# Kernel optimization log

Measured on AMD Instinct MI355X. Metric: run time of the kernel, lower is better.

## Reference

```python
import jax, jax.numpy as jnp
import numpy as np


def setup_inputs() -> dict:
    key = jax.random.key(0)
    ks = jax.random.split(key, 8)
    N, DIN, DOUT = 8192, 1024, 1024
    s = 1.0 / np.sqrt(DIN)
    return {
        "gAB": jax.random.normal(ks[0], (N, DIN), dtype=jnp.float32),
        "gAG": jax.random.normal(ks[1], (N, DIN), dtype=jnp.float32),
        "Wab": jax.random.normal(ks[2], (DIN, DOUT), dtype=jnp.float32) * s,
        "Wag": jax.random.normal(ks[3], (DIN, DOUT), dtype=jnp.float32) * s,
        "bab": jax.random.normal(ks[4], (DOUT,), dtype=jnp.float32) * 0.01,
        "bag": jax.random.normal(ks[5], (DOUT,), dtype=jnp.float32) * 0.01,
        "sAB": jax.random.normal(ks[6], (N, DOUT), dtype=jnp.float32),
        "sAG": jax.random.normal(ks[7], (N, DOUT), dtype=jnp.float32),
    }


def reference(gAB, gAG, Wab, Wag, bab, bag, sAB, sAG) -> jnp.ndarray:
    # project() per encoder (Linear): [N, DIN] @ [DIN, DOUT] + b
    pAB = gAB @ Wab + bab  # [N, DOUT]
    pAG = gAG @ Wag + bag  # [N, DOUT]
    # torch.diag(pAB @ pAG.T) == row-wise dot product (avoids O(N^2 d) waste)
    h1 = jnp.sum(pAB * pAG, axis=1, keepdims=True)  # [N, 1]
    h2 = jnp.sum(sAB * sAG, axis=1, keepdims=True)  # [N, 1]
    # mean over concatenated (h1, h2) columns, keepdim=True
    h = jnp.mean(jnp.concatenate([h1, h2], axis=1), axis=1, keepdims=True)  # [N, 1]
    return h
```

## Files before the change

kernel.cpp:

```cpp
#include <hip/hip_runtime.h>
#include <hip/hip_bf16.h>
#include <stdint.h>

typedef __attribute__((ext_vector_type(8))) short bf16x8;
typedef __attribute__((ext_vector_type(4))) float f32x4;

#define DIN 1024
#define NROWS 8192

__device__ __forceinline__ unsigned short f2bf(float f) {
    union { float f; unsigned u; } v; v.f = f;
    unsigned r = v.u + 0x7FFFu + ((v.u >> 16) & 1u);
    return (unsigned short)(r >> 16);
}

__device__ __forceinline__ int fswz(int r) { return (r ^ (r >> 2)) & 3; }

__device__ __forceinline__ size_t swz_byte(int R, int col) {
    return ((size_t)R * DIN + (col & ~31)) * 2 + (size_t)((((col >> 3) & 3) ^ fswz(R)) << 4) + (size_t)((col & 7) * 2);
}

__device__ __forceinline__ void gload_lds16(const void* g, void* l) {
    __builtin_amdgcn_global_load_lds(
        (const __attribute__((address_space(1))) unsigned*)g,
        (__attribute__((address_space(3))) unsigned*)l, 16, 0, 0);
}

__global__ __launch_bounds__(256) void prep_kernel(const float* __restrict__ Wab,
                                                   const float* __restrict__ Wag,
                                                   const float* __restrict__ bab,
                                                   const float* __restrict__ bag,
                                                   float* __restrict__ ws_f,
                                                   unsigned short* __restrict__ Whab,
                                                   unsigned short* __restrict__ Whag) {
    int b = blockIdx.x;
    int wave = threadIdx.x >> 6, lane = threadIdx.x & 63;
    if (b == 256) {
        if (wave == 0) {
            float acc = 0.f;
            for (int j = lane; j < DIN; j += 64) acc += bab[j] * bag[j];
            for (int off = 32; off; off >>= 1) acc += __shfl_xor(acc, off);
            if (lane == 0) ws_f[2048] = acc;
        }
        return;
    }
    int r = b * 4 + wave;
    int fr = fswz(r);
    {
        const float* wrow = Wab + (size_t)r * DIN;
        char* hrow = (char*)Whab + (size_t)r * DIN * 2;
        float acc = 0.f;
#pragma unroll
        for (int it = 0; it < 4; ++it) {
            int col = it * 256 + lane * 4;
            float4 w = *reinterpret_cast<const float4*>(wrow + col);
            float4 bv = *reinterpret_cast<const float4*>(bag + col);
            acc += w.x * bv.x + w.y * bv.y + w.z * bv.z + w.w * bv.w;
            ushort4 h; h.x = f2bf(w.x); h.y = f2bf(w.y); h.z = f2bf(w.z); h.w = f2bf(w.w);
            *reinterpret_cast<ushort4*>(hrow + (col & ~31) * 2 + ((((col >> 3) & 3) ^ fr) << 4) + (col & 7) * 2) = h;
        }
        for (int off = 32; off; off >>= 1) acc += __shfl_xor(acc, off);
        if (lane == 0) ws_f[r] = acc;
    }
    {
        const float* wrow = Wag + (size_t)r * DIN;
        char* hrow = (char*)Whag + (size_t)r * DIN * 2;
        float acc = 0.f;
#pragma unroll
        for (int it = 0; it < 4; ++it) {
            int col = it * 256 + lane * 4;
            float4 w = *reinterpret_cast<const float4*>(wrow + col);
            float4 bv = *reinterpret_cast<const float4*>(bab + col);
            acc += w.x * bv.x + w.y * bv.y + w.z * bv.z + w.w * bv.w;
            ushort4 h; h.x = f2bf(w.x); h.y = f2bf(w.y); h.z = f2bf(w.z); h.w = f2bf(w.w);
            *reinterpret_cast<ushort4*>(hrow + (col & ~31) * 2 + ((((col >> 3) & 3) ^ fr) << 4) + (col & 7) * 2) = h;
        }
        for (int off = 32; off; off >>= 1) acc += __shfl_xor(acc, off);
        if (lane == 0) ws_f[1024 + r] = acc;
    }
}

__global__ __launch_bounds__(512) void mt_kernel(const unsigned short* __restrict__ Whag,
                                                 const unsigned short* __restrict__ Whab,
                                                 unsigned short* __restrict__ Mt) {
    __shared__ unsigned short sm[2][2][2][2048];
    int tid = threadIdx.x;
    int wave = tid >> 6, grp = wave >> 2, w4 = wave & 3;
    int lane = tid & 63, kg = lane >> 4, cl = lane & 15;
    int wr = w4 >> 1, wc = w4 & 1;
    int br = blockIdx.x >> 4, bc = blockIdx.x & 15;
    int u = tid & 255, urow = u >> 2, uchunk = u & 3;

    const char* Abase = (const char*)Whag + ((size_t)(br * 64 + urow) * DIN + grp * 512) * 2 + uchunk * 16;
    const char* Bbase = (const char*)Whab + ((size_t)(bc * 64 + urow) * DIN + grp * 512) * 2 + uchunk * 16;

    int offA[2], offB[2];
#pragma unroll
    for (int m = 0; m < 2; ++m) { int row = wr * 32 + m * 16 + cl; offA[m] = row * 32 + ((kg ^ fswz(row)) << 3); }
#pragma unroll
    for (int n = 0; n < 2; ++n) { int row = wc * 32 + n * 16 + cl; offB[n] = row * 32 + ((kg ^ fswz(row)) << 3); }

    f32x4 acc[2][2] = {};
    gload_lds16(Abase, &sm[grp][0][0][u * 8]);
    gload_lds16(Bbase, &sm[grp][0][1][u * 8]);
    __syncthreads();
    for (int t = 0; t < 16; ++t) {
        int p = t & 1;
        if (t < 15) {
            gload_lds16(Abase + (t + 1) * 64, &sm[grp][p ^ 1][0][u * 8]);
            gload_lds16(Bbase + (t + 1) * 64, &sm[grp][p ^ 1][1][u * 8]);
        }
        bf16x8 af[2], bfr[2];
#pragma unroll
        for (int m = 0; m < 2; ++m) af[m] = *reinterpret_cast<const bf16x8*>(&sm[grp][p][0][offA[m]]);
#pragma unroll
        for (int n = 0; n < 2; ++n) bfr[n] = *reinterpret_cast<const bf16x8*>(&sm[grp][p][1][offB[n]]);
#pragma unroll
        for (int m = 0; m < 2; ++m)
#pragma unroll
            for (int n = 0; n < 2; ++n)
                acc[m][n] = __builtin_amdgcn_mfma_f32_16x16x32_bf16(af[m], bfr[n], acc[m][n], 0, 0, 0);
        __syncthreads();
    }
    float* red = (float*)sm;
    if (grp == 1) {
#pragma unroll
        for (int m = 0; m < 2; ++m)
#pragma unroll
            for (int n = 0; n < 2; ++n)
#pragma unroll
                for (int j = 0; j < 4; ++j)
                    red[(wr * 32 + m * 16 + kg * 4 + j) * 68 + wc * 32 + n * 16 + cl] = acc[m][n][j];
    }
    __syncthreads();
    if (grp == 0) {
#pragma unroll
        for (int m = 0; m < 2; ++m)
#pragma unroll
            for (int n = 0; n < 2; ++n)
#pragma unroll
                for (int j = 0; j < 4; ++j) {
                    int rl = wr * 32 + m * 16 + kg * 4 + j, cll = wc * 32 + n * 16 + cl;
                    float v = acc[m][n][j] + red[rl * 68 + cll];
                    int R = br * 64 + rl, C = bc * 64 + cll;
                    *(unsigned short*)((char*)Mt + swz_byte(R, C & ~3) + (C & 3) * 2) = f2bf(v);
                }
    }
}

template <int KSPLIT>
__global__ __launch_bounds__(256, 4) void gemm_fused(const float* __restrict__ gAB,
                                                     const float* __restrict__ gAG,
                                                     const float* __restrict__ sAB,
                                                     const float* __restrict__ sAG,
                                                     const unsigned short* __restrict__ Mt,
                                                     const float* __restrict__ ws_f,
                                                     float* __restrict__ out) {
    __shared__ unsigned short lds_a[2][128 * 32];
    __shared__ unsigned short lds_b[2][128 * 32];
    constexpr int KLEN = DIN / KSPLIT;
    constexpr int NSTEP = KLEN / 32;
    int b = blockIdx.x;
    int x = b & 7, s = b >> 3;
    int rblk = x + 8 * (s & 7);
    int u2 = s >> 3;
    int ks = u2 & (KSPLIT - 1);
    int cblk = u2 / KSPLIT;
    int tid = threadIdx.x, wave = tid >> 6, lane = tid & 63;
    int wr = wave >> 1, wc = wave & 1;
    int kg = lane >> 4, cl = lane & 15;
    int row0 = rblk * 128, col0 = cblk * 128;

    int offA[4], offB[4];
#pragma unroll
    for (int m = 0; m < 4; ++m) { int row = wr * 64 + m * 16 + cl; offA[m] = row * 32 + ((kg ^ fswz(row)) << 3); }
#pragma unroll
    for (int n = 0; n < 4; ++n) { int row = wc * 64 + n * 16 + cl; offB[n] = row * 32 + ((kg ^ fswz(row)) << 3); }

    size_t kofs = (size_t)(ks * KLEN);
    const char* Bb = (const char*)Mt + ((size_t)col0 * DIN + kofs) * 2;
    int u0 = tid, u1 = tid + 256;
    size_t b0 = (size_t)(u0 >> 2) * (DIN * 2) + (u0 & 3) * 16;
    size_t b1 = (size_t)(u1 >> 2) * (DIN * 2) + (u1 & 3) * 16;
    const float* Abase = gAB + (size_t)row0 * DIN + kofs;

    f32x4 acc[4][4] = {};
    float4 ra[4];

    gload_lds16(Bb + b0, (char*)&lds_b[0][0] + u0 * 16);
    gload_lds16(Bb + b1, (char*)&lds_b[0][0] + u1 * 16);
#pragma unroll
    for (int it = 0; it < 4; ++it) {
        int u = tid + it * 256;
        ra[it] = *reinterpret_cast<const float4*>(Abase + (size_t)(u >> 3) * DIN + (u & 7) * 4);
    }
#pragma unroll
    for (int it = 0; it < 4; ++it) {
        int u = tid + it * 256, row = u >> 3, c4 = u & 7;
        ushort4 h; h.x = f2bf(ra[it].x); h.y = f2bf(ra[it].y); h.z = f2bf(ra[it].z); h.w = f2bf(ra[it].w);
        *reinterpret_cast<ushort4*>((char*)&lds_a[0][0] + row * 64 + ((((c4 >> 1) ^ fswz(row))) << 4) + (c4 & 1) * 8) = h;
    }
    __syncthreads();

    for (int t = 0; t < NSTEP; ++t) {
        int p = t & 1;
        if (t < NSTEP - 1) {
#pragma unroll
            for (int it = 0; it < 4; ++it) {
                int u = tid + it * 256;
                ra[it] = *reinterpret_cast<const float4*>(Abase + (size_t)(u >> 3) * DIN + (t + 1) * 32 + (u & 7) * 4);
            }
            gload_lds16(Bb + b0 + (t + 1) * 64, (char*)&lds_b[p ^ 1][0] + u0 * 16);
            gload_lds16(Bb + b1 + (t + 1) * 64, (char*)&lds_b[p ^ 1][0] + u1 * 16);
        }
        bf16x8 af[4], bfr[4];
#pragma unroll
        for (int m = 0; m < 4; ++m) af[m] = *reinterpret_cast<const bf16x8*>(&lds_a[p][offA[m]]);
#pragma unroll
        for (int n = 0; n < 4; ++n) bfr[n] = *reinterpret_cast<const bf16x8*>(&lds_b[p][offB[n]]);
#pragma unroll
        for (int m = 0; m < 4; ++m)
#pragma unroll
            for (int n = 0; n < 4; ++n)
                acc[m][n] = __builtin_amdgcn_mfma_f32_16x16x32_bf16(af[m], bfr[n], acc[m][n], 0, 0, 0);
        if (t < NSTEP - 1) {
#pragma unroll
            for (int it = 0; it < 4; ++it) {
                int u = tid + it * 256, row = u >> 3, c4 = u & 7;
                ushort4 h; h.x = f2bf(ra[it].x); h.y = f2bf(ra[it].y); h.z = f2bf(ra[it].z); h.w = f2bf(ra[it].w);
                *reinterpret_cast<ushort4*>((char*)&lds_a[p ^ 1][0] + row * 64 + ((((c4 >> 1) ^ fswz(row))) << 4) + (c4 & 1) * 8) = h;
            }
        }
        __syncthreads();
    }

    const float* vab = ws_f;
    const float* vag = ws_f + 1024;
    float cbias = ws_f[2048];
#pragma unroll
    for (int m = 0; m < 4; ++m)
#pragma unroll
        for (int j = 0; j < 4; ++j) {
            int row = row0 + wr * 64 + m * 16 + kg * 4 + j;
            const float* gr = gAG + (size_t)row * DIN;
            float t = 0.f;
#pragma unroll
            for (int n = 0; n < 4; ++n) {
                int col = col0 + wc * 64 + n * 16 + cl;
                float addv = (ks == 0) ? vag[col] : 0.f;
                t += gr[col] * (acc[m][n][j] + addv);
            }
            if (ks == 0) {
                const float* gar = gAB + (size_t)row * DIN;
                const float* sar = sAB + (size_t)row * DIN;
                const float* sgr = sAG + (size_t)row * DIN;
#pragma unroll
                for (int n = 0; n < 4; ++n) {
                    int col = col0 + wc * 64 + n * 16 + cl;
                    t += gar[col] * vab[col] + sar[col] * sgr[col];
                }
            }
            t += __shfl_xor(t, 1);
            t += __shfl_xor(t, 2);
            t += __shfl_xor(t, 4);
            t += __shfl_xor(t, 8);
            if (cl == 0) {
                float add = (ks == 0 && cblk == 0 && wc == 0) ? cbias : 0.f;
                atomicAdd(out + row, 0.5f * (t + add));
            }
        }
}

extern "C" void kernel_launch(void* const* d_in, const int* in_sizes, int n_in,
                              void* d_out, int out_size, void* d_ws, size_t ws_size,
                              hipStream_t stream) {
    const float* gAB = (const float*)d_in[0];
    const float* gAG = (const float*)d_in[1];
    const float* Wab = (const float*)d_in[2];
    const float* Wag = (const float*)d_in[3];
    const float* bab = (const float*)d_in[4];
    const float* bag = (const float*)d_in[5];
    const float* sAB = (const float*)d_in[6];
    const float* sAG = (const float*)d_in[7];
    float* out = (float*)d_out;

    float* ws_f = (float*)d_ws;
    char* base = (char*)d_ws + 16384;
    unsigned short* Mt = (unsigned short*)base;
    unsigned short* Whag = (unsigned short*)(base + (size_t)2 * 1024 * 1024);
    unsigned short* Whab = (unsigned short*)(base + (size_t)4 * 1024 * 1024);

    hipMemsetAsync(d_out, 0, (size_t)out_size * sizeof(float), stream);
    prep_kernel<<<257, 256, 0, stream>>>(Wab, Wag, bab, bag, ws_f, Whab, Whag);
    mt_kernel<<<256, 512, 0, stream>>>(Whag, Whab, Mt);
    gemm_fused<2><<<1024, 256, 0, stream>>>(gAB, gAG, sAB, sAG, Mt, ws_f, out);
}
```

Baseline: 70.45 us.

## Split row-dot and bias terms into dedicated blocks of a merged GEMM kernel

Adds 256 extra blocks to the fused GEMM launch. Each extra block streams rows of gAB, sAB and sAG with coalesced float4 loads and computes the sAB·sAG dot plus the gAB·vab bias term per row. The GEMM epilogue no longer does these scattered per-lane loads for the ks==0 tiles, which removes load imbalance between the K-split halves and cuts strided global reads. Occupancy hint raised from 4 to 5 blocks per SM; this risks register spills, and the streaming blocks compete for bandwidth with the GEMM blocks.

```diff
diff --git a/kernel.cpp b/kernel.cpp
--- a/kernel.cpp
+++ b/kernel.cpp
@@ -148,25 +148,56 @@
     }
 }
 
-template <int KSPLIT>
-__global__ __launch_bounds__(256, 4) void gemm_fused(const float* __restrict__ gAB,
-                                                     const float* __restrict__ gAG,
-                                                     const float* __restrict__ sAB,
-                                                     const float* __restrict__ sAG,
-                                                     const unsigned short* __restrict__ Mt,
-                                                     const float* __restrict__ ws_f,
-                                                     float* __restrict__ out) {
+__global__ __launch_bounds__(256, 5) void mega_kernel(const float* __restrict__ gAB,
+                                                      const float* __restrict__ gAG,
+                                                      const float* __restrict__ sAB,
+                                                      const float* __restrict__ sAG,
+                                                      const unsigned short* __restrict__ Mt,
+                                                      const float* __restrict__ ws_f,
+                                                      float* __restrict__ out) {
     __shared__ unsigned short lds_a[2][128 * 32];
     __shared__ unsigned short lds_b[2][128 * 32];
+    int b = blockIdx.x;
+    int tid = threadIdx.x, wave = tid >> 6, lane = tid & 63;
+
+    if (b < 256) {
+        float cbias = ws_f[2048];
+        float4 vb[4];
+#pragma unroll
+        for (int cc = 0; cc < 4; ++cc)
+            vb[cc] = *reinterpret_cast<const float4*>(ws_f + cc * 256 + lane * 4);
+        int row_base = b * 32 + wave * 8;
+        for (int rr = 0; rr < 8; ++rr) {
+            int row = row_base + rr;
+            const float* ga = gAB + (size_t)row * DIN;
+            const float* sa = sAB + (size_t)row * DIN;
+            const float* sg = sAG + (size_t)row * DIN;
+            float acc = 0.f;
+#pragma unroll
+            for (int cc = 0; cc < 4; ++cc) {
+                int col = cc * 256 + lane * 4;
+                float4 a = *reinterpret_cast<const float4*>(ga + col);
+                float4 x = *reinterpret_cast<const float4*>(sa + col);
+                float4 y = *reinterpret_cast<const float4*>(sg + col);
+                acc += x.x * y.x + x.y * y.y + x.z * y.z + x.w * y.w;
+                acc += a.x * vb[cc].x + a.y * vb[cc].y + a.z * vb[cc].z + a.w * vb[cc].w;
+            }
+#pragma unroll
+            for (int off = 32; off; off >>= 1) acc += __shfl_xor(acc, off);
+            if (lane == 0) atomicAdd(out + row, 0.5f * (acc + cbias));
+        }
+        return;
+    }
+
+    constexpr int KSPLIT = 2;
     constexpr int KLEN = DIN / KSPLIT;
     constexpr int NSTEP = KLEN / 32;
-    int b = blockIdx.x;
-    int x = b & 7, s = b >> 3;
+    int g = b - 256;
+    int x = g & 7, s = g >> 3;
     int rblk = x + 8 * (s & 7);
     int u2 = s >> 3;
     int ks = u2 & (KSPLIT - 1);
     int cblk = u2 / KSPLIT;
-    int tid = threadIdx.x, wave = tid >> 6, lane = tid & 63;
     int wr = wave >> 1, wc = wave & 1;
     int kg = lane >> 4, cl = lane & 15;
     int row0 = rblk * 128, col0 = cblk * 128;
@@ -234,9 +265,7 @@
         __syncthreads();
     }
 
-    const float* vab = ws_f;
     const float* vag = ws_f + 1024;
-    float cbias = ws_f[2048];
 #pragma unroll
     for (int m = 0; m < 4; ++m)
 #pragma unroll
@@ -250,24 +279,11 @@
                 float addv = (ks == 0) ? vag[col] : 0.f;
                 t += gr[col] * (acc[m][n][j] + addv);
             }
-            if (ks == 0) {
-                const float* gar = gAB + (size_t)row * DIN;
-                const float* sar = sAB + (size_t)row * DIN;
-                const float* sgr = sAG + (size_t)row * DIN;
-#pragma unroll
-                for (int n = 0; n < 4; ++n) {
-                    int col = col0 + wc * 64 + n * 16 + cl;
-                    t += gar[col] * vab[col] + sar[col] * sgr[col];
-                }
-            }
             t += __shfl_xor(t, 1);
             t += __shfl_xor(t, 2);
             t += __shfl_xor(t, 4);
             t += __shfl_xor(t, 8);
-            if (cl == 0) {
-                float add = (ks == 0 && cblk == 0 && wc == 0) ? cbias : 0.f;
-                atomicAdd(out + row, 0.5f * (t + add));
-            }
+            if (cl == 0) atomicAdd(out + row, 0.5f * t);
         }
 }
 
@@ -293,5 +309,5 @@
     hipMemsetAsync(d_out, 0, (size_t)out_size * sizeof(float), stream);
     prep_kernel<<<257, 256, 0, stream>>>(Wab, Wag, bab, bag, ws_f, Whab, Whag);
     mt_kernel<<<256, 512, 0, stream>>>(Whag, Whab, Mt);
-    gemm_fused<2><<<1024, 256, 0, stream>>>(gAB, gAG, sAB, sAG, Mt, ws_f, out);
-}
+    mega_kernel<<<1280, 256, 0, stream>>>(gAB, gAG, sAB, sAG, Mt, ws_f, out);
+}
```

Result: slower. 112.1 us (+59.1%).

## Fuse bf16 weight conversion into Mt GEMM and move bias/sAB·sAG terms into main loop

Applied to the files above, without the earlier changes.

Drops the separate bf16 copies of Wab/Wag: prep now only computes bias-projection vectors, and mt_kernel reads fp32 weights, converts them in registers and writes them to LDS. The main GEMM switches Mt to an 8-way XOR swizzle with a matching B staging pattern. It computes gAB·vab during the A conversion and sAB·sAG per column slice inside the K loop, reduced through LDS atomics. This removes the epilogue's scattered strided loads of gAB/sAB/sAG and the extra weight-conversion traffic. In exchange, the main loop carries more per-iteration global loads and the kernel adds LDS atomics.

```diff
diff --git a/kernel.cpp b/kernel.cpp
--- a/kernel.cpp
+++ b/kernel.cpp
@@ -14,10 +14,10 @@
     return (unsigned short)(r >> 16);
 }
 
-__device__ __forceinline__ int fswz(int r) { return (r ^ (r >> 2)) & 3; }
-
-__device__ __forceinline__ size_t swz_byte(int R, int col) {
-    return ((size_t)R * DIN + (col & ~31)) * 2 + (size_t)((((col >> 3) & 3) ^ fswz(R)) << 4) + (size_t)((col & 7) * 2);
+__device__ __forceinline__ size_t swz8_byte(int R, int c) {
+    return ((size_t)R * DIN + (size_t)(c & ~63)) * 2
+         + (size_t)(((((c >> 3) & 7) ^ (R & 7)) << 4))
+         + (size_t)((c & 7) * 2);
 }
 
 __device__ __forceinline__ void gload_lds16(const void* g, void* l) {
@@ -30,9 +30,7 @@
                                                    const float* __restrict__ Wag,
                                                    const float* __restrict__ bab,
                                                    const float* __restrict__ bag,
-                                                   float* __restrict__ ws_f,
-                                                   unsigned short* __restrict__ Whab,
-                                                   unsigned short* __restrict__ Whag) {
+                                                   float* __restrict__ ws_f) {
     int b = blockIdx.x;
     int wave = threadIdx.x >> 6, lane = threadIdx.x & 63;
     if (b == 256) {
@@ -45,43 +43,26 @@
         return;
     }
     int r = b * 4 + wave;
-    int fr = fswz(r);
-    {
-        const float* wrow = Wab + (size_t)r * DIN;
-        char* hrow = (char*)Whab + (size_t)r * DIN * 2;
-        float acc = 0.f;
-#pragma unroll
-        for (int it = 0; it < 4; ++it) {
-            int col = it * 256 + lane * 4;
-            float4 w = *reinterpret_cast<const float4*>(wrow + col);
-            float4 bv = *reinterpret_cast<const float4*>(bag + col);
-            acc += w.x * bv.x + w.y * bv.y + w.z * bv.z + w.w * bv.w;
-            ushort4 h; h.x = f2bf(w.x); h.y = f2bf(w.y); h.z = f2bf(w.z); h.w = f2bf(w.w);
-            *reinterpret_cast<ushort4*>(hrow + (col & ~31) * 2 + ((((col >> 3) & 3) ^ fr) << 4) + (col & 7) * 2) = h;
-        }
-        for (int off = 32; off; off >>= 1) acc += __shfl_xor(acc, off);
-        if (lane == 0) ws_f[r] = acc;
-    }
-    {
-        const float* wrow = Wag + (size_t)r * DIN;
-        char* hrow = (char*)Whag + (size_t)r * DIN * 2;
-        float acc = 0.f;
-#pragma unroll
-        for (int it = 0; it < 4; ++it) {
-            int col = it * 256 + lane * 4;
-            float4 w = *reinterpret_cast<const float4*>(wrow + col);
-            float4 bv = *reinterpret_cast<const float4*>(bab + col);
-            acc += w.x * bv.x + w.y * bv.y + w.z * bv.z + w.w * bv.w;
-            ushort4 h; h.x = f2bf(w.x); h.y = f2bf(w.y); h.z = f2bf(w.z); h.w = f2bf(w.w);
-            *reinterpret_cast<ushort4*>(hrow + (col & ~31) * 2 + ((((col >> 3) & 3) ^ fr) << 4) + (col & 7) * 2) = h;
-        }
-        for (int off = 32; off; off >>= 1) acc += __shfl_xor(acc, off);
-        if (lane == 0) ws_f[1024 + r] = acc;
-    }
-}
-
-__global__ __launch_bounds__(512) void mt_kernel(const unsigned short* __restrict__ Whag,
-                                                 const unsigned short* __restrict__ Whab,
+    const float* w1r = Wab + (size_t)r * DIN;
+    const float* w2r = Wag + (size_t)r * DIN;
+    float a1 = 0.f, a2 = 0.f;
+#pragma unroll
+    for (int it = 0; it < 4; ++it) {
+        int col = it * 256 + lane * 4;
+        float4 w1 = *reinterpret_cast<const float4*>(w1r + col);
+        float4 bg = *reinterpret_cast<const float4*>(bag + col);
+        float4 w2 = *reinterpret_cast<const float4*>(w2r + col);
+        float4 bb = *reinterpret_cast<const float4*>(bab + col);
+        a1 += w1.x * bg.x + w1.y * bg.y + w1.z * bg.z + w1.w * bg.w;
+        a2 += w2.x * bb.x + w2.y * bb.y + w2.z * bb.z + w2.w * bb.w;
+    }
+#pragma unroll
+    for (int off = 32; off; off >>= 1) { a1 += __shfl_xor(a1, off); a2 += __shfl_xor(a2, off); }
+    if (lane == 0) { ws_f[r] = a1; ws_f[1024 + r] = a2; }
+}
+
+__global__ __launch_bounds__(512) void mt_kernel(const float* __restrict__ Wag_,
+                                                 const float* __restrict__ Wab_,
                                                  unsigned short* __restrict__ Mt) {
     __shared__ unsigned short sm[2][2][2][2048];
     int tid = threadIdx.x;
@@ -89,27 +70,40 @@
     int lane = tid & 63, kg = lane >> 4, cl = lane & 15;
     int wr = w4 >> 1, wc = w4 & 1;
     int br = blockIdx.x >> 4, bc = blockIdx.x & 15;
-    int u = tid & 255, urow = u >> 2, uchunk = u & 3;
-
-    const char* Abase = (const char*)Whag + ((size_t)(br * 64 + urow) * DIN + grp * 512) * 2 + uchunk * 16;
-    const char* Bbase = (const char*)Whab + ((size_t)(bc * 64 + urow) * DIN + grp * 512) * 2 + uchunk * 16;
+    int u = tid & 255;
 
     int offA[2], offB[2];
 #pragma unroll
-    for (int m = 0; m < 2; ++m) { int row = wr * 32 + m * 16 + cl; offA[m] = row * 32 + ((kg ^ fswz(row)) << 3); }
-#pragma unroll
-    for (int n = 0; n < 2; ++n) { int row = wc * 32 + n * 16 + cl; offB[n] = row * 32 + ((kg ^ fswz(row)) << 3); }
+    for (int m = 0; m < 2; ++m) { int row = wr * 32 + m * 16 + cl; offA[m] = row * 32 + ((kg ^ (row & 3)) << 3); }
+#pragma unroll
+    for (int n = 0; n < 2; ++n) { int row = wc * 32 + n * 16 + cl; offB[n] = row * 32 + ((kg ^ (row & 3)) << 3); }
+
+    float4 raA[2], raB[2];
+#define LOADMT(t)                                                                          \
+    _Pragma("unroll")                                                                      \
+    for (int it = 0; it < 2; ++it) {                                                       \
+        int un = u + it * 256, rowu = un >> 3, c4 = un & 7;                                \
+        raA[it] = *reinterpret_cast<const float4*>(Wag_ + (size_t)(br * 64 + rowu) * DIN + grp * 512 + (t) * 32 + c4 * 4); \
+        raB[it] = *reinterpret_cast<const float4*>(Wab_ + (size_t)(bc * 64 + rowu) * DIN + grp * 512 + (t) * 32 + c4 * 4); \
+    }
+#define WRITEMT(buf, t)                                                                    \
+    _Pragma("unroll")                                                                      \
+    for (int it = 0; it < 2; ++it) {                                                       \
+        int un = u + it * 256, rowu = un >> 3, c4 = un & 7;                                \
+        int slot = rowu * 32 + ((((c4 >> 1) ^ (rowu & 3))) << 3) + (c4 & 1) * 4;           \
+        ushort4 hA; hA.x = f2bf(raA[it].x); hA.y = f2bf(raA[it].y); hA.z = f2bf(raA[it].z); hA.w = f2bf(raA[it].w); \
+        *reinterpret_cast<ushort4*>(&sm[grp][buf][0][slot]) = hA;                          \
+        ushort4 hB; hB.x = f2bf(raB[it].x); hB.y = f2bf(raB[it].y); hB.z = f2bf(raB[it].z); hB.w = f2bf(raB[it].w); \
+        *reinterpret_cast<ushort4*>(&sm[grp][buf][1][slot]) = hB;                          \
+    }
 
     f32x4 acc[2][2] = {};
-    gload_lds16(Abase, &sm[grp][0][0][u * 8]);
-    gload_lds16(Bbase, &sm[grp][0][1][u * 8]);
+    LOADMT(0);
+    WRITEMT(0, 0);
     __syncthreads();
     for (int t = 0; t < 16; ++t) {
         int p = t & 1;
-        if (t < 15) {
-            gload_lds16(Abase + (t + 1) * 64, &sm[grp][p ^ 1][0][u * 8]);
-            gload_lds16(Bbase + (t + 1) * 64, &sm[grp][p ^ 1][1][u * 8]);
-        }
+        if (t < 15) { LOADMT(t + 1); }
         bf16x8 af[2], bfr[2];
 #pragma unroll
         for (int m = 0; m < 2; ++m) af[m] = *reinterpret_cast<const bf16x8*>(&sm[grp][p][0][offA[m]]);
@@ -120,8 +114,11 @@
 #pragma unroll
             for (int n = 0; n < 2; ++n)
                 acc[m][n] = __builtin_amdgcn_mfma_f32_16x16x32_bf16(af[m], bfr[n], acc[m][n], 0, 0, 0);
+        if (t < 15) { WRITEMT(p ^ 1, t + 1); }
         __syncthreads();
     }
+#undef LOADMT
+#undef WRITEMT
     float* red = (float*)sm;
     if (grp == 1) {
 #pragma unroll
@@ -143,100 +140,125 @@
                     int rl = wr * 32 + m * 16 + kg * 4 + j, cll = wc * 32 + n * 16 + cl;
                     float v = acc[m][n][j] + red[rl * 68 + cll];
                     int R = br * 64 + rl, C = bc * 64 + cll;
-                    *(unsigned short*)((char*)Mt + swz_byte(R, C & ~3) + (C & 3) * 2) = f2bf(v);
+                    *(unsigned short*)((char*)Mt + swz8_byte(R, C)) = f2bf(v);
                 }
     }
 }
 
-template <int KSPLIT>
-__global__ __launch_bounds__(256, 4) void gemm_fused(const float* __restrict__ gAB,
-                                                     const float* __restrict__ gAG,
-                                                     const float* __restrict__ sAB,
-                                                     const float* __restrict__ sAG,
-                                                     const unsigned short* __restrict__ Mt,
-                                                     const float* __restrict__ ws_f,
-                                                     float* __restrict__ out) {
+__global__ __launch_bounds__(256, 4) void fused_kernel(const float* __restrict__ gAB,
+                                                       const float* __restrict__ gAG,
+                                                       const float* __restrict__ sAB,
+                                                       const float* __restrict__ sAG,
+                                                       const unsigned short* __restrict__ Mt,
+                                                       const float* __restrict__ ws_f,
+                                                       float* __restrict__ out) {
     __shared__ unsigned short lds_a[2][128 * 32];
     __shared__ unsigned short lds_b[2][128 * 32];
-    constexpr int KLEN = DIN / KSPLIT;
-    constexpr int NSTEP = KLEN / 32;
+    constexpr int NSTEP = 16;
     int b = blockIdx.x;
     int x = b & 7, s = b >> 3;
     int rblk = x + 8 * (s & 7);
     int u2 = s >> 3;
-    int ks = u2 & (KSPLIT - 1);
-    int cblk = u2 / KSPLIT;
+    int ks = u2 & 1;
+    int cblk = u2 >> 1;
     int tid = threadIdx.x, wave = tid >> 6, lane = tid & 63;
     int wr = wave >> 1, wc = wave & 1;
     int kg = lane >> 4, cl = lane & 15;
     int row0 = rblk * 128, col0 = cblk * 128;
+    int hcol0 = ((cblk << 1) | ks) * 64;
 
     int offA[4], offB[4];
 #pragma unroll
-    for (int m = 0; m < 4; ++m) { int row = wr * 64 + m * 16 + cl; offA[m] = row * 32 + ((kg ^ fswz(row)) << 3); }
-#pragma unroll
-    for (int n = 0; n < 4; ++n) { int row = wc * 64 + n * 16 + cl; offB[n] = row * 32 + ((kg ^ fswz(row)) << 3); }
-
-    size_t kofs = (size_t)(ks * KLEN);
-    const char* Bb = (const char*)Mt + ((size_t)col0 * DIN + kofs) * 2;
-    int u0 = tid, u1 = tid + 256;
-    size_t b0 = (size_t)(u0 >> 2) * (DIN * 2) + (u0 & 3) * 16;
-    size_t b1 = (size_t)(u1 >> 2) * (DIN * 2) + (u1 & 3) * 16;
-    const float* Abase = gAB + (size_t)row0 * DIN + kofs;
+    for (int m = 0; m < 4; ++m) { int row = wr * 64 + m * 16 + cl; offA[m] = row * 64 + ((kg ^ (row & 3)) << 4); }
+#pragma unroll
+    for (int n = 0; n < 4; ++n) { int row = wc * 64 + n * 16 + cl; offB[n] = row * 64 + ((kg ^ (row & 3)) << 4); }
+
+    const float* Af = gAB + (size_t)row0 * DIN + ks * 512;
+    const char* Bb = (const char*)Mt + ((size_t)col0 * DIN + ks * 512) * 2;
+    const float* vab = ws_f;
+    const float* vag = ws_f + 1024;
+
+    const float* saRow = sAB + (size_t)(row0 + (tid >> 1)) * DIN + hcol0 + (tid & 1) * 2;
+    const float* sgRow = sAG + (size_t)(row0 + (tid >> 1)) * DIN + hcol0 + (tid & 1) * 2;
 
     f32x4 acc[4][4] = {};
     float4 ra[4];
-
-    gload_lds16(Bb + b0, (char*)&lds_b[0][0] + u0 * 16);
-    gload_lds16(Bb + b1, (char*)&lds_b[0][0] + u1 * 16);
-#pragma unroll
-    for (int it = 0; it < 4; ++it) {
-        int u = tid + it * 256;
-        ra[it] = *reinterpret_cast<const float4*>(Abase + (size_t)(u >> 3) * DIN + (u & 7) * 4);
-    }
-#pragma unroll
-    for (int it = 0; it < 4; ++it) {
-        int u = tid + it * 256, row = u >> 3, c4 = u & 7;
-        ushort4 h; h.x = f2bf(ra[it].x); h.y = f2bf(ra[it].y); h.z = f2bf(ra[it].z); h.w = f2bf(ra[it].w);
-        *reinterpret_cast<ushort4*>((char*)&lds_a[0][0] + row * 64 + ((((c4 >> 1) ^ fswz(row))) << 4) + (c4 & 1) * 8) = h;
-    }
+    float tacc[4] = {0.f, 0.f, 0.f, 0.f};
+    float hacc = 0.f;
+
+#define LOADA(t)                                                                           \
+    _Pragma("unroll")                                                                      \
+    for (int it = 0; it < 4; ++it) {                                                       \
+        int un = tid + it * 256;                                                           \
+        ra[it] = *reinterpret_cast<const float4*>(Af + (size_t)(un >> 3) * DIN + (t) * 32 + (un & 7) * 4); \
+    }
+#define WRITEA(buf, t) do {                                                                \
+    float4 vv = *reinterpret_cast<const float4*>(vab + ks * 512 + (t) * 32 + (tid & 7) * 4); \
+    _Pragma("unroll")                                                                      \
+    for (int it = 0; it < 4; ++it) {                                                       \
+        int un = tid + it * 256, row_ = un >> 3, c4 = un & 7;                              \
+        if (cblk == 0)                                                                     \
+            tacc[it] += ra[it].x * vv.x + ra[it].y * vv.y + ra[it].z * vv.z + ra[it].w * vv.w; \
+        ushort4 h; h.x = f2bf(ra[it].x); h.y = f2bf(ra[it].y); h.z = f2bf(ra[it].z); h.w = f2bf(ra[it].w); \
+        *reinterpret_cast<ushort4*>((char*)&lds_a[buf][0] + row_ * 64 +                    \
+                                    ((((c4 >> 1) ^ (row_ & 3))) << 4) + (c4 & 1) * 8) = h; \
+    } } while (0)
+#define STAGE_B(buf, t)                                                                    \
+    _Pragma("unroll")                                                                      \
+    for (int it = 0; it < 2; ++it) {                                                       \
+        int un = tid + it * 256, row_ = un >> 2, s_ = un & 3;                              \
+        int pg = ((((t) & 1) << 2) ^ (row_ & 4)) | s_;                                     \
+        gload_lds16(Bb + (size_t)row_ * 2048 + ((t) >> 1) * 128 + pg * 16,                 \
+                    (char*)&lds_b[buf][0] + un * 16);                                      \
+    }
+
+    STAGE_B(0, 0);
+    LOADA(0);
+    WRITEA(0, 0);
     __syncthreads();
 
     for (int t = 0; t < NSTEP; ++t) {
         int p = t & 1;
         if (t < NSTEP - 1) {
-#pragma unroll
-            for (int it = 0; it < 4; ++it) {
-                int u = tid + it * 256;
-                ra[it] = *reinterpret_cast<const float4*>(Abase + (size_t)(u >> 3) * DIN + (t + 1) * 32 + (u & 7) * 4);
-            }
-            gload_lds16(Bb + b0 + (t + 1) * 64, (char*)&lds_b[p ^ 1][0] + u0 * 16);
-            gload_lds16(Bb + b1 + (t + 1) * 64, (char*)&lds_b[p ^ 1][0] + u1 * 16);
+            STAGE_B(p ^ 1, t + 1);
+            LOADA(t + 1);
         }
-        bf16x8 af[4], bfr[4];
-#pragma unroll
-        for (int m = 0; m < 4; ++m) af[m] = *reinterpret_cast<const bf16x8*>(&lds_a[p][offA[m]]);
-#pragma unroll
-        for (int n = 0; n < 4; ++n) bfr[n] = *reinterpret_cast<const bf16x8*>(&lds_b[p][offB[n]]);
-#pragma unroll
-        for (int m = 0; m < 4; ++m)
+        float2 sa2 = *reinterpret_cast<const float2*>(saRow + t * 4);
+        float2 sg2 = *reinterpret_cast<const float2*>(sgRow + t * 4);
+        bf16x8 bfr[4];
+#pragma unroll
+        for (int n = 0; n < 4; ++n) bfr[n] = *reinterpret_cast<const bf16x8*>((char*)&lds_b[p][0] + offB[n]);
+#pragma unroll
+        for (int m = 0; m < 4; ++m) {
+            bf16x8 af = *reinterpret_cast<const bf16x8*>((char*)&lds_a[p][0] + offA[m]);
 #pragma unroll
             for (int n = 0; n < 4; ++n)
-                acc[m][n] = __builtin_amdgcn_mfma_f32_16x16x32_bf16(af[m], bfr[n], acc[m][n], 0, 0, 0);
-        if (t < NSTEP - 1) {
-#pragma unroll
-            for (int it = 0; it < 4; ++it) {
-                int u = tid + it * 256, row = u >> 3, c4 = u & 7;
-                ushort4 h; h.x = f2bf(ra[it].x); h.y = f2bf(ra[it].y); h.z = f2bf(ra[it].z); h.w = f2bf(ra[it].w);
-                *reinterpret_cast<ushort4*>((char*)&lds_a[p ^ 1][0] + row * 64 + ((((c4 >> 1) ^ fswz(row))) << 4) + (c4 & 1) * 8) = h;
-            }
+                acc[m][n] = __builtin_amdgcn_mfma_f32_16x16x32_bf16(af, bfr[n], acc[m][n], 0, 0, 0);
         }
+        hacc += sa2.x * sg2.x + sa2.y * sg2.y;
+        if (t < NSTEP - 1) { WRITEA(p ^ 1, t + 1); }
         __syncthreads();
     }
-
-    const float* vab = ws_f;
-    const float* vag = ws_f + 1024;
-    float cbias = ws_f[2048];
+#undef LOADA
+#undef WRITEA
+#undef STAGE_B
+
+    float* rowacc = (float*)&lds_a[0][0];
+    if (tid < 128) rowacc[tid] = 0.f;
+    __syncthreads();
+    if (cblk == 0) {
+#pragma unroll
+        for (int it = 0; it < 4; ++it)
+            atomicAdd(&rowacc[(tid >> 3) + it * 32], tacc[it]);
+    }
+    atomicAdd(&rowacc[tid >> 1], hacc);
+    __syncthreads();
+    if (tid < 128) {
+        float v = rowacc[tid];
+        if (cblk == 0 && ks == 0) v += ws_f[2048];
+        atomicAdd(out + row0 + tid, 0.5f * v);
+    }
+
 #pragma unroll
     for (int m = 0; m < 4; ++m)
 #pragma unroll
@@ -250,24 +272,11 @@
                 float addv = (ks == 0) ? vag[col] : 0.f;
                 t += gr[col] * (acc[m][n][j] + addv);
             }
-            if (ks == 0) {
-                const float* gar = gAB + (size_t)row * DIN;
-                const float* sar = sAB + (size_t)row * DIN;
-                const float* sgr = sAG + (size_t)row * DIN;
-#pragma unroll
-                for (int n = 0; n < 4; ++n) {
-                    int col = col0 + wc * 64 + n * 16 + cl;
-                    t += gar[col] * vab[col] + sar[col] * sgr[col];
-                }
-            }
             t += __shfl_xor(t, 1);
             t += __shfl_xor(t, 2);
             t += __shfl_xor(t, 4);
             t += __shfl_xor(t, 8);
-            if (cl == 0) {
-                float add = (ks == 0 && cblk == 0 && wc == 0) ? cbias : 0.f;
-                atomicAdd(out + row, 0.5f * (t + add));
-            }
+            if (cl == 0) atomicAdd(out + row, 0.5f * t);
         }
 }
 
@@ -285,13 +294,10 @@
     float* out = (float*)d_out;
 
     float* ws_f = (float*)d_ws;
-    char* base = (char*)d_ws + 16384;
-    unsigned short* Mt = (unsigned short*)base;
-    unsigned short* Whag = (unsigned short*)(base + (size_t)2 * 1024 * 1024);
-    unsigned short* Whab = (unsigned short*)(base + (size_t)4 * 1024 * 1024);
+    unsigned short* Mt = (unsigned short*)((char*)d_ws + 16384);
 
     hipMemsetAsync(d_out, 0, (size_t)out_size * sizeof(float), stream);
-    prep_kernel<<<257, 256, 0, stream>>>(Wab, Wag, bab, bag, ws_f, Whab, Whag);
-    mt_kernel<<<256, 512, 0, stream>>>(Whag, Whab, Mt);
-    gemm_fused<2><<<1024, 256, 0, stream>>>(gAB, gAG, sAB, sAG, Mt, ws_f, out);
-}
+    prep_kernel<<<257, 256, 0, stream>>>(Wab, Wag, bab, bag, ws_f);
+    mt_kernel<<<256, 512, 0, stream>>>(Wag, Wab, Mt);
+    fused_kernel<<<1024, 256, 0, stream>>>(gAB, gAG, sAB, sAG, Mt, ws_f, out);
+}
```

Result: slower. 133.9 us (+90.1%).
